# Optimization experiments

Hardware: AMD Instinct MI355X
Metric: run time of the kernel (lower is better)

The kernel has to match this reference:

```python
import jax, jax.numpy as jnp
import numpy as np

VOCAB_SIZES = [100003, 100019, 100043, 100049, 100057, 100069, 100103, 100109,
               100129, 100151, 100153, 100169, 100183, 100189, 100193, 100207]
OFFSETS = np.cumsum([0] + VOCAB_SIZES[:-1]).astype(np.int32)  # per-head offsets into shared table
B, S, G, C = 2, 2048, 4, 2048        # batch, seq, hc_mult branches, base_emb_dim
H, DH = 16, 64                        # total hash heads, dim_per_head
ENGRAM_DIM = H * DH                   # 1024 = num_orders * dim_per_ngram
K, DIL = 4, 3                         # conv kernel_size, dilation = max_ngram_size


def setup_inputs() -> dict:
  key = jax.random.key(0)
  ks = jax.random.split(key, 8)
  total_vocab = sum(VOCAB_SIZES)
  return {
      "hidden_states": jax.random.normal(ks[0], (B, S, G, C), jnp.float32),
      "hash_input_ids": jax.random.randint(ks[1], (B, S, H), 0, min(VOCAB_SIZES), jnp.int32),
      "emb_table": jax.random.normal(ks[2], (total_vocab, DH), jnp.float32) * 0.02,
      "key_w": jax.random.normal(ks[3], (G, ENGRAM_DIM, C), jnp.float32) / np.sqrt(ENGRAM_DIM),
      "key_b": jnp.zeros((G, C), jnp.float32),
      "k_scale": jnp.ones((G, C), jnp.float32) + 0.02 * jax.random.normal(ks[4], (G, C), jnp.float32),
      "q_scale": jnp.ones((G, C), jnp.float32) + 0.02 * jax.random.normal(ks[5], (G, C), jnp.float32),
      "value_w": jax.random.normal(ks[6], (ENGRAM_DIM, C), jnp.float32) / np.sqrt(ENGRAM_DIM),
      "value_b": jnp.zeros((C,), jnp.float32),
      "conv_scale": jnp.ones((G, C), jnp.float32),
      "conv_w": jax.random.normal(ks[7], (K, G * C), jnp.float32) * 0.25,  # depthwise taps
  }


def _rmsnorm(x, scale, eps):
  var = jnp.mean(jnp.square(x), axis=-1, keepdims=True)
  return x * jax.lax.rsqrt(var + eps) * scale


def reference(hidden_states, hash_input_ids, emb_table, key_w, key_b,
              k_scale, q_scale, value_w, value_b, conv_scale, conv_w):
  # 1. Retrieve: offset-shifted multi-head embedding gather
  ids = hash_input_ids + jnp.asarray(OFFSETS)            # (B,S,H)
  emb = emb_table[ids].reshape(B, S, ENGRAM_DIM)         # (B,S,H*DH)
  # 2. Gate: per-branch key projections + RMSNorms, signed-sqrt sigmoid gate
  keys = jnp.einsum('bse,geo->bsgo', emb, key_w) + key_b  # (B,S,G,C)
  k = _rmsnorm(keys, k_scale, 1e-6)
  q = _rmsnorm(hidden_states, q_scale, 1e-6)
  qk = jnp.einsum('bsgc,bsgc->bsg', q, k) / jnp.sqrt(jnp.float32(C))
  gate_logits = jnp.sqrt(jnp.maximum(jnp.abs(qk), 1e-6)) * jnp.sign(qk)
  gates = jax.nn.sigmoid(gate_logits)                    # (B,S,G)
  value = emb @ value_w + value_b                        # (B,S,C)
  v = gates[..., None] * value[:, :, None, :]            # (B,S,G,C)
  # 3. Mix: ShortConv = SiLU(depthwise causal dilated Conv1D(RMSNorm(v)))
  xn = _rmsnorm(v, conv_scale, 1e-5).reshape(B, S, G * C)
  pad = (K - 1) * DIL                                    # causal left pad = 9
  xp = jnp.pad(xn, ((0, 0), (pad, 0), (0, 0)))
  y = sum(xp[:, j * DIL:j * DIL + S, :] * conv_w[j] for j in range(K))
  y = jax.nn.silu(y).reshape(B, S, G, C)
  return v + y
```

## Files before the change

### kernel.cpp

```cpp
#include <hip/hip_runtime.h>
#include <cstdint>
#include <cstddef>

typedef __attribute__((ext_vector_type(8))) __bf16 bf16x8;
typedef __attribute__((ext_vector_type(4))) float f32x4;
typedef __attribute__((ext_vector_type(4))) unsigned short u16x4;
typedef __attribute__((ext_vector_type(8))) unsigned short u16x8;

static constexpr int Bz = 2, Sz = 2048, Gz = 4, Cz = 2048;
static constexpr int Hh = 16, EDz = 1024;
static constexpr int Tz = Bz * Sz;
static constexpr int NALL = Gz * Cz + Cz;

__constant__ int OFF16[16] = {0, 100003, 200022, 300065, 400114, 500171, 600240,
                              700343, 800452, 900581, 1000732, 1100885, 1201054,
                              1301237, 1401426, 1501619};

__device__ __forceinline__ float bf2f(unsigned short s) {
  union { unsigned u; float f; } x; x.u = ((unsigned)s) << 16; return x.f;
}
__device__ __forceinline__ unsigned short f2bf(float f) {
  union { float f; unsigned u; } x; x.f = f;
  unsigned r = x.u + 0x7fff + ((x.u >> 16) & 1);
  return (unsigned short)(r >> 16);
}

__global__ __launch_bounds__(256) void k_prep0(float* __restrict__ sums) {
  int i = blockIdx.x * 256 + threadIdx.x;
  if (i < 53248) sums[i] = 0.f;
}

__global__ __launch_bounds__(256) void k_prepw(const float* __restrict__ key_w,
                                               const float* __restrict__ value_w,
                                               unsigned short* __restrict__ Wt) {
  __shared__ float tile[32][33];
  const int mat = blockIdx.y;
  const int ot = blockIdx.x & 63, kt = blockIdx.x >> 6;
  const float* src = (mat < 4) ? (key_w + (size_t)mat * EDz * Cz) : value_w;
  const int tx = threadIdx.x & 31, ty = threadIdx.x >> 5;
#pragma unroll
  for (int i = 0; i < 4; i++)
    tile[ty + i * 8][tx] = src[(size_t)(kt * 32 + ty + i * 8) * Cz + ot * 32 + tx];
  __syncthreads();
#pragma unroll
  for (int i = 0; i < 4; i++)
    Wt[(size_t)(mat * Cz + ot * 32 + ty + i * 8) * EDz + kt * 32 + tx] =
        f2bf(tile[tx][ty + i * 8]);
}

__global__ __launch_bounds__(256) void k_gather(const int* __restrict__ ids,
                                                const float* __restrict__ table,
                                                unsigned short* __restrict__ emb) {
  const int t = blockIdx.x;
  const int tid = threadIdx.x;
  const int h = tid >> 4;
  const int d = (tid & 15) * 4;
  const long row = (long)(ids[t * Hh + h] + OFF16[h]);
  f32x4 v = *reinterpret_cast<const f32x4*>(table + row * 64 + d);
  u16x4 o;
#pragma unroll
  for (int i = 0; i < 4; i++) o[i] = f2bf(v[i]);
  *reinterpret_cast<u16x4*>(emb + (size_t)t * EDz + tid * 4) = o;
}

#define GEMM_BAR  asm volatile("s_barrier" ::: "memory")
#define GEMM_V4   asm volatile("s_waitcnt vmcnt(4)" ::: "memory")

__global__ __launch_bounds__(512, 2) void k_gemm8f(const unsigned short* __restrict__ A,
                                                   const unsigned short* __restrict__ Bw,
                                                   const float* __restrict__ hidden,
                                                   const float* __restrict__ key_b,
                                                   const float* __restrict__ value_b,
                                                   const float* __restrict__ q_scale,
                                                   const float* __restrict__ k_scale,
                                                   float* __restrict__ sums,
                                                   unsigned short* __restrict__ vbuf) {
  __shared__ unsigned short s_lds[65536];
  char* lds_c = (char*)s_lds;

  const int tid = threadIdx.x;
  const int wid = tid >> 6, lane = tid & 63;
  const int wr = wid >> 2, wc = wid & 3;

  const int bid = blockIdx.x;
  const int swz = (bid & 7) * 80 + (bid >> 3);
  const int bm = swz / 40, bn = swz % 40;
  const int m0 = bm * 256, n0 = bn * 256;

  int rq[2], kq[2];
#pragma unroll
  for (int q = 0; q < 2; q++) {
    int x = q * 8192 + wid * 1024 + lane * 16;
    int y = x ^ (((x >> 9) & 1) << 5);
    rq[q] = ((y >> 11) & 7) * 16 + ((y >> 6) & 15);
    kq[q] = ((y >> 10) & 1) * 32 + ((y >> 1) & 31);
  }
  const int rdb = (((lane & 15) << 6) + ((lane >> 4) << 4)) ^ (((lane >> 3) & 1) << 5);

  const unsigned short* Arow0 = A + (size_t)m0 * EDz;
  const unsigned short* Arow1 = A + (size_t)(m0 + 128) * EDz;
  const unsigned short* Brow0 = Bw + (size_t)n0 * EDz;
  const unsigned short* Brow1 = Bw + (size_t)(n0 + 128) * EDz;

  auto STAGE = [&](const unsigned short* grow, int ldsOff, int kt) {
#pragma unroll
    for (int q = 0; q < 2; q++) {
      const unsigned short* src = grow + (size_t)rq[q] * EDz + kt * 64 + kq[q];
      __builtin_amdgcn_global_load_lds(
          (const __attribute__((address_space(1))) void*)src,
          (__attribute__((address_space(3))) void*)(lds_c + ldsOff + q * 8192 + wid * 1024),
          16, 0, 0);
    }
  };

  f32x4 acc[8][4] = {};
  bf16x8 Af[4][2], Bl[2][2], Bh[2][2];

  auto RD_A = [&](int buf, int msel) {
    const char* p = lds_c + buf * 32768 + wr * 16384 + rdb;
#pragma unroll
    for (int m = 0; m < 4; m++)
#pragma unroll
      for (int ks = 0; ks < 2; ks++)
        Af[m][ks] = *reinterpret_cast<const bf16x8*>(p + (msel * 4 + m) * 2048 + ks * 1024);
  };
  auto RD_B = [&](int buf, int nsel, bf16x8 (&Bf)[2][2]) {
    const char* p = lds_c + 65536 + buf * 32768 + (wc >> 1) * 16384 + (wc & 1) * 8192 + rdb;
#pragma unroll
    for (int n = 0; n < 2; n++)
#pragma unroll
      for (int ks = 0; ks < 2; ks++)
        Bf[n][ks] = *reinterpret_cast<const bf16x8*>(p + (nsel * 2 + n) * 2048 + ks * 1024);
  };
  auto MM = [&](int msel, int nsel, bf16x8 (&Bf)[2][2]) {
    __builtin_amdgcn_s_setprio(1);
#pragma unroll
    for (int m = 0; m < 4; m++)
#pragma unroll
      for (int n = 0; n < 2; n++)
#pragma unroll
        for (int ks = 0; ks < 2; ks++)
          acc[msel * 4 + m][nsel * 2 + n] = __builtin_amdgcn_mfma_f32_16x16x32_bf16(
              Af[m][ks], Bf[n][ks], acc[msel * 4 + m][nsel * 2 + n], 0, 0, 0);
    __builtin_amdgcn_s_setprio(0);
  };

  STAGE(Arow0, 0,             0);
  STAGE(Arow1, 16384,         0);
  STAGE(Brow0, 65536,         0);
  STAGE(Brow1, 65536 + 16384, 0);
  STAGE(Brow0, 65536 + 32768,         1);
  STAGE(Brow1, 65536 + 32768 + 16384, 1);
  GEMM_V4;
  GEMM_BAR;

  for (int i = 0; i < 8; ++i) {
    const int o  = 2 * i + 1;
    const int t2 = (2 * i + 2 > 15) ? 15 : 2 * i + 2;
    const int t3 = (2 * i + 3 > 15) ? 15 : 2 * i + 3;
    RD_A(0, 0); RD_B(0, 0, Bl);
    STAGE(Arow0, 32768, o);
    GEMM_BAR; MM(0, 0, Bl); GEMM_BAR;
    RD_B(0, 1, Bh);
    STAGE(Arow1, 32768 + 16384, o);
    GEMM_BAR; MM(0, 1, Bh); GEMM_BAR;
    RD_A(0, 1);
    STAGE(Brow0, 65536, t2);
    GEMM_BAR; MM(1, 0, Bl); GEMM_BAR;
    STAGE(Brow1, 65536 + 16384, t2);
    GEMM_V4;
    GEMM_BAR; MM(1, 1, Bh); GEMM_BAR;
    RD_A(1, 0); RD_B(1, 0, Bl);
    STAGE(Arow0, 0, t2);
    GEMM_BAR; MM(0, 0, Bl); GEMM_BAR;
    RD_B(1, 1, Bh);
    STAGE(Arow1, 16384, t2);
    GEMM_BAR; MM(0, 1, Bh); GEMM_BAR;
    RD_A(1, 1);
    STAGE(Brow0, 65536 + 32768, t3);
    GEMM_BAR; MM(1, 0, Bl); GEMM_BAR;
    STAGE(Brow1, 65536 + 32768 + 16384, t3);
    GEMM_V4;
    GEMM_BAR; MM(1, 1, Bh); GEMM_BAR;
  }

  float* sum_q2  = sums;
  float* sum_k2  = sums + 16384;
  float* sum_qwk = sums + 32768;
  float* sum_v2  = sums + 49152;

  if (n0 < 8192) {
    const int g = n0 >> 11;
#pragma unroll
    for (int mrep = 0; mrep < 8; mrep++) {
      const int rowb = wr * 128 + mrep * 16 + (lane >> 4) * 4;
#pragma unroll
      for (int nrep = 0; nrep < 4; nrep++) {
        const int coll = wc * 64 + nrep * 16 + (lane & 15);
        const float kb = key_b[n0 + coll];
#pragma unroll
        for (int t = 0; t < 4; t++) {
          const int row = rowb + t;
          const int addr = (row * 512 + coll * 2) ^ ((row & 15) << 4);
          *reinterpret_cast<unsigned short*>(lds_c + addr) =
              f2bf(acc[mrep][nrep][t] + kb);
        }
      }
    }
    __syncthreads();
    const int wrow = wid * 32;
    const int lrow = lane >> 3;
    const int lsub = lane & 7;
#pragma unroll
    for (int rr = 0; rr < 4; rr++) {
      const int row = wrow + rr * 8 + lrow;
      const int grow = m0 + row;
      const float* hp = hidden + (size_t)grow * 8192 + n0;
      float a_k2 = 0.f, a_qwk = 0.f, a_q2 = 0.f;
#pragma unroll
      for (int c8 = 0; c8 < 4; c8++) {
        const int lc = c8 * 64 + lsub * 8;
        const int addr = (row * 512 + lc * 2) ^ ((row & 15) << 4);
        bf16x8 k8 = *reinterpret_cast<const bf16x8*>(lds_c + addr);
        f32x4 h0 = *reinterpret_cast<const f32x4*>(hp + lc);
        f32x4 h1 = *reinterpret_cast<const f32x4*>(hp + lc + 4);
        f32x4 qs0 = *reinterpret_cast<const f32x4*>(q_scale + n0 + lc);
        f32x4 qs1 = *reinterpret_cast<const f32x4*>(q_scale + n0 + lc + 4);
        f32x4 ks0 = *reinterpret_cast<const f32x4*>(k_scale + n0 + lc);
        f32x4 ks1 = *reinterpret_cast<const f32x4*>(k_scale + n0 + lc + 4);
#pragma unroll
        for (int i = 0; i < 8; i++) {
          const float kf = (float)k8[i];
          const float hf = (i < 4) ? h0[i] : h1[i - 4];
          const float wf = ((i < 4) ? qs0[i] : qs1[i - 4]) *
                           ((i < 4) ? ks0[i] : ks1[i - 4]);
          a_k2  += kf * kf;
          a_qwk += kf * hf * wf;
          a_q2  += hf * hf;
        }
      }
#pragma unroll
      for (int msk = 1; msk <= 4; msk <<= 1) {
        a_k2  += __shfl_xor(a_k2, msk);
        a_qwk += __shfl_xor(a_qwk, msk);
        a_q2  += __shfl_xor(a_q2, msk);
      }
      if (lsub == 0) {
        const int idx = grow * 4 + g;
        atomicAdd(&sum_k2[idx], a_k2);
        atomicAdd(&sum_qwk[idx], a_qwk);
        atomicAdd(&sum_q2[idx], a_q2);
      }
    }
  } else {
#pragma unroll
    for (int mrep = 0; mrep < 8; mrep++) {
      const int rowb = m0 + wr * 128 + mrep * 16 + (lane >> 4) * 4;
      float av2[4] = {0.f, 0.f, 0.f, 0.f};
#pragma unroll
      for (int nrep = 0; nrep < 4; nrep++) {
        const int vcol = n0 - 8192 + wc * 64 + nrep * 16 + (lane & 15);
        const float vb = value_b[vcol];
#pragma unroll
        for (int t = 0; t < 4; t++) {
          const float v = acc[mrep][nrep][t] + vb;
          av2[t] += v * v;
          vbuf[(size_t)(rowb + t) * 2048 + vcol] = f2bf(v);
        }
      }
#pragma unroll
      for (int t = 0; t < 4; t++) {
        float a = av2[t];
#pragma unroll
        for (int msk = 1; msk <= 8; msk <<= 1) a += __shfl_xor(a, msk);
        if ((lane & 15) == 0) atomicAdd(&sum_v2[rowb + t], a);
      }
    }
  }
}

__global__ __launch_bounds__(256) void k_gatefin(const float* __restrict__ sums,
                                                 float* __restrict__ gates,
                                                 float* __restrict__ rstd) {
  const int i = blockIdx.x * 256 + threadIdx.x;
  const float* sum_q2  = sums;
  const float* sum_k2  = sums + 16384;
  const float* sum_qwk = sums + 32768;
  const float* sum_v2  = sums + 49152;
  const int t = i >> 2;
  const float invC = 1.f / 2048.f;
  const float inv_sqrtC = 0.02209708691f;
  float rqv = rsqrtf(sum_q2[i] * invC + 1e-6f);
  float rkv = rsqrtf(sum_k2[i] * invC + 1e-6f);
  float qk = sum_qwk[i] * rqv * rkv * inv_sqrtC;
  float l = sqrtf(fmaxf(fabsf(qk), 1e-6f));
  l = (qk < 0.f) ? -l : l;
  float gate = 1.f / (1.f + expf(-l));
  gates[i] = gate;
  rstd[i] = rsqrtf(gate * gate * (sum_v2[t] * invC) + 1e-5f);
}

__global__ __launch_bounds__(256) void k_conv(const unsigned short* __restrict__ vbuf,
                                              const float* __restrict__ gates,
                                              const float* __restrict__ rstd,
                                              const float* __restrict__ conv_scale,
                                              const float* __restrict__ conv_w,
                                              float* __restrict__ out) {
  const int th = threadIdx.x;
  const int r = blockIdx.x % 3, seg = blockIdx.x / 3;
  const int bg = blockIdx.y;
  const int b = bg >> 2, g = bg & 3;
  const int c8 = th * 8;
  const int ch = g * Cz + c8;

  float cs[8], w0[8], w1[8], w2[8], w3[8];
#pragma unroll
  for (int q = 0; q < 2; q++) {
    f32x4 a = *reinterpret_cast<const f32x4*>(conv_scale + ch + q * 4);
    f32x4 t0 = *reinterpret_cast<const f32x4*>(conv_w + 0 * 8192 + ch + q * 4);
    f32x4 t1 = *reinterpret_cast<const f32x4*>(conv_w + 1 * 8192 + ch + q * 4);
    f32x4 t2 = *reinterpret_cast<const f32x4*>(conv_w + 2 * 8192 + ch + q * 4);
    f32x4 t3 = *reinterpret_cast<const f32x4*>(conv_w + 3 * 8192 + ch + q * 4);
#pragma unroll
    for (int i = 0; i < 4; i++) {
      cs[q * 4 + i] = a[i];
      w0[q * 4 + i] = t0[i]; w1[q * 4 + i] = t1[i];
      w2[q * 4 + i] = t2[i]; w3[q * 4 + i] = t3[i];
    }
  }

  const int s_begin = seg * 64, s_end = s_begin + 64;
  const int s0 = s_begin + ((r - s_begin) % 3 + 3) % 3;

  float p1[8], p2[8], p3[8];
  auto ldxn = [&](int s, float* dst) {
    if (s < 0) {
#pragma unroll
      for (int i = 0; i < 8; i++) dst[i] = 0.f;
      return;
    }
    const int t = b * Sz + s;
    const float grs = gates[t * 4 + g] * rstd[t * 4 + g];
    u16x8 raw = *reinterpret_cast<const u16x8*>(vbuf + (size_t)t * 2048 + c8);
#pragma unroll
    for (int i = 0; i < 8; i++) dst[i] = bf2f(raw[i]) * grs * cs[i];
  };
  ldxn(s0 - 3, p1); ldxn(s0 - 6, p2); ldxn(s0 - 9, p3);

  for (int s = s0; s < s_end; s += 3) {
    const int t = b * Sz + s;
    const float gate = gates[t * 4 + g];
    const float rsc = rstd[t * 4 + g];
    u16x8 raw = *reinterpret_cast<const u16x8*>(vbuf + (size_t)t * 2048 + c8);
    f32x4 o0, o1;
#pragma unroll
    for (int i = 0; i < 8; i++) {
      float v = bf2f(raw[i]) * gate;
      float xn = v * rsc * cs[i];
      float y = w3[i] * xn + w2[i] * p1[i] + w1[i] * p2[i] + w0[i] * p3[i];
      float sy = y / (1.f + expf(-y));
      float ov = v + sy;
      if (i < 4) o0[i] = ov; else o1[i - 4] = ov;
      p3[i] = p2[i]; p2[i] = p1[i]; p1[i] = xn;
    }
    float* op = out + (size_t)t * (Gz * Cz) + ch;
    *reinterpret_cast<f32x4*>(op) = o0;
    *reinterpret_cast<f32x4*>(op + 4) = o1;
  }
}

extern "C" void kernel_launch(void* const* d_in, const int* in_sizes, int n_in,
                              void* d_out, int out_size, void* d_ws, size_t ws_size,
                              hipStream_t stream) {
  const float* hidden     = (const float*)d_in[0];
  const int*   hashids    = (const int*)d_in[1];
  const float* table      = (const float*)d_in[2];
  const float* key_w      = (const float*)d_in[3];
  const float* key_b      = (const float*)d_in[4];
  const float* k_scale    = (const float*)d_in[5];
  const float* q_scale    = (const float*)d_in[6];
  const float* value_w    = (const float*)d_in[7];
  const float* value_b    = (const float*)d_in[8];
  const float* conv_scale = (const float*)d_in[9];
  const float* conv_w     = (const float*)d_in[10];
  float* out = (float*)d_out;
  char* ws = (char*)d_ws;

  unsigned short* emb  = (unsigned short*)(ws + 0);
  unsigned short* Wt   = (unsigned short*)(ws + 8388608);
  unsigned short* vbuf = (unsigned short*)(ws + 29360128);
  float* sums  = (float*)(ws + 46137344);
  float* gates = (float*)(ws + 46350336);
  float* rstd  = (float*)(ws + 46415872);

  k_prep0<<<dim3(208), dim3(256), 0, stream>>>(sums);
  k_prepw<<<dim3(2048, 5), dim3(256), 0, stream>>>(key_w, value_w, Wt);
  k_gather<<<dim3(Tz), dim3(256), 0, stream>>>(hashids, table, emb);
  k_gemm8f<<<dim3(640), dim3(512), 0, stream>>>(emb, Wt, hidden, key_b, value_b,
                                                q_scale, k_scale, sums, vbuf);
  k_gatefin<<<dim3(64), dim3(256), 0, stream>>>(sums, gates, rstd);
  k_conv<<<dim3(96, 8), dim3(256), 0, stream>>>(vbuf, gates, rstd, conv_scale, conv_w, out);
}
```

Before: 202.0 us.

## Fuse prep kernels into one launch and fold gate finalize into conv

Merges the sums-zeroing, weight transpose/convert and embedding gather kernels into a single launch that picks its role by block index. It also removes the separate gate-finalize kernel: each conv block now computes the gates and rstd values for its 64-row segment plus the 9-row causal halo into shared memory. The goal is to cut launch overhead and the intermediate gates/rstd round trip through global memory. In exchange, conv blocks recompute the gate values for halo rows and for each of the three residue blocks, and a block-wide barrier is added before the conv loop.

```diff
diff --git a/kernel.cpp b/kernel.cpp
--- a/kernel.cpp
+++ b/kernel.cpp
@@ -25,42 +25,44 @@
   return (unsigned short)(r >> 16);
 }
 
-__global__ __launch_bounds__(256) void k_prep0(float* __restrict__ sums) {
-  int i = blockIdx.x * 256 + threadIdx.x;
-  if (i < 53248) sums[i] = 0.f;
-}
-
-__global__ __launch_bounds__(256) void k_prepw(const float* __restrict__ key_w,
-                                               const float* __restrict__ value_w,
-                                               unsigned short* __restrict__ Wt) {
+__global__ __launch_bounds__(256) void k_prep(const float* __restrict__ key_w,
+                                              const float* __restrict__ value_w,
+                                              const float* __restrict__ table,
+                                              const int* __restrict__ ids,
+                                              unsigned short* __restrict__ Wt,
+                                              unsigned short* __restrict__ emb,
+                                              float* __restrict__ sums) {
+  const int b = blockIdx.x;
   __shared__ float tile[32][33];
-  const int mat = blockIdx.y;
-  const int ot = blockIdx.x & 63, kt = blockIdx.x >> 6;
-  const float* src = (mat < 4) ? (key_w + (size_t)mat * EDz * Cz) : value_w;
-  const int tx = threadIdx.x & 31, ty = threadIdx.x >> 5;
-#pragma unroll
-  for (int i = 0; i < 4; i++)
-    tile[ty + i * 8][tx] = src[(size_t)(kt * 32 + ty + i * 8) * Cz + ot * 32 + tx];
-  __syncthreads();
-#pragma unroll
-  for (int i = 0; i < 4; i++)
-    Wt[(size_t)(mat * Cz + ot * 32 + ty + i * 8) * EDz + kt * 32 + tx] =
-        f2bf(tile[tx][ty + i * 8]);
-}
-
-__global__ __launch_bounds__(256) void k_gather(const int* __restrict__ ids,
-                                                const float* __restrict__ table,
-                                                unsigned short* __restrict__ emb) {
-  const int t = blockIdx.x;
-  const int tid = threadIdx.x;
-  const int h = tid >> 4;
-  const int d = (tid & 15) * 4;
-  const long row = (long)(ids[t * Hh + h] + OFF16[h]);
-  f32x4 v = *reinterpret_cast<const f32x4*>(table + row * 64 + d);
-  u16x4 o;
-#pragma unroll
-  for (int i = 0; i < 4; i++) o[i] = f2bf(v[i]);
-  *reinterpret_cast<u16x4*>(emb + (size_t)t * EDz + tid * 4) = o;
+  if (b < 10240) {
+    const int mat = b / 2048;
+    const int inner = b - mat * 2048;
+    const int ot = inner & 63, kt = inner >> 6;
+    const float* src = (mat < 4) ? (key_w + (size_t)mat * EDz * Cz) : value_w;
+    const int tx = threadIdx.x & 31, ty = threadIdx.x >> 5;
+#pragma unroll
+    for (int i = 0; i < 4; i++)
+      tile[ty + i * 8][tx] = src[(size_t)(kt * 32 + ty + i * 8) * Cz + ot * 32 + tx];
+    __syncthreads();
+#pragma unroll
+    for (int i = 0; i < 4; i++)
+      Wt[(size_t)(mat * Cz + ot * 32 + ty + i * 8) * EDz + kt * 32 + tx] =
+          f2bf(tile[tx][ty + i * 8]);
+  } else if (b < 14336) {
+    const int t = b - 10240;
+    const int tid = threadIdx.x;
+    const int h = tid >> 4;
+    const int d = (tid & 15) * 4;
+    const long row = (long)(ids[t * Hh + h] + OFF16[h]);
+    f32x4 v = *reinterpret_cast<const f32x4*>(table + row * 64 + d);
+    u16x4 o;
+#pragma unroll
+    for (int i = 0; i < 4; i++) o[i] = f2bf(v[i]);
+    *reinterpret_cast<u16x4*>(emb + (size_t)t * EDz + tid * 4) = o;
+  } else {
+    const int i = (b - 14336) * 256 + threadIdx.x;
+    if (i < 53248) sums[i] = 0.f;
+  }
 }
 
 #define GEMM_BAR  asm volatile("s_barrier" ::: "memory")
@@ -279,30 +281,8 @@
   }
 }
 
-__global__ __launch_bounds__(256) void k_gatefin(const float* __restrict__ sums,
-                                                 float* __restrict__ gates,
-                                                 float* __restrict__ rstd) {
-  const int i = blockIdx.x * 256 + threadIdx.x;
-  const float* sum_q2  = sums;
-  const float* sum_k2  = sums + 16384;
-  const float* sum_qwk = sums + 32768;
-  const float* sum_v2  = sums + 49152;
-  const int t = i >> 2;
-  const float invC = 1.f / 2048.f;
-  const float inv_sqrtC = 0.02209708691f;
-  float rqv = rsqrtf(sum_q2[i] * invC + 1e-6f);
-  float rkv = rsqrtf(sum_k2[i] * invC + 1e-6f);
-  float qk = sum_qwk[i] * rqv * rkv * inv_sqrtC;
-  float l = sqrtf(fmaxf(fabsf(qk), 1e-6f));
-  l = (qk < 0.f) ? -l : l;
-  float gate = 1.f / (1.f + expf(-l));
-  gates[i] = gate;
-  rstd[i] = rsqrtf(gate * gate * (sum_v2[t] * invC) + 1e-5f);
-}
-
 __global__ __launch_bounds__(256) void k_conv(const unsigned short* __restrict__ vbuf,
-                                              const float* __restrict__ gates,
-                                              const float* __restrict__ rstd,
+                                              const float* __restrict__ sums,
                                               const float* __restrict__ conv_scale,
                                               const float* __restrict__ conv_w,
                                               float* __restrict__ out) {
@@ -312,6 +292,29 @@
   const int b = bg >> 2, g = bg & 3;
   const int c8 = th * 8;
   const int ch = g * Cz + c8;
+  const int s_begin = seg * 64, s_end = s_begin + 64;
+
+  __shared__ float g_lds[73], r_lds[73];
+  if (th < 73) {
+    const int s = s_begin - 9 + th;
+    if (s >= 0) {
+      const int t = b * Sz + s;
+      const int idx = t * 4 + g;
+      const float invC = 1.f / 2048.f;
+      const float inv_sqrtC = 0.02209708691f;
+      float rqv = rsqrtf(sums[idx] * invC + 1e-6f);
+      float rkv = rsqrtf(sums[16384 + idx] * invC + 1e-6f);
+      float qk = sums[32768 + idx] * rqv * rkv * inv_sqrtC;
+      float l = sqrtf(fmaxf(fabsf(qk), 1e-6f));
+      l = (qk < 0.f) ? -l : l;
+      float gate = 1.f / (1.f + expf(-l));
+      g_lds[th] = gate;
+      r_lds[th] = rsqrtf(gate * gate * (sums[49152 + t] * invC) + 1e-5f);
+    } else {
+      g_lds[th] = 0.f; r_lds[th] = 0.f;
+    }
+  }
+  __syncthreads();
 
   float cs[8], w0[8], w1[8], w2[8], w3[8];
 #pragma unroll
@@ -329,7 +332,6 @@
     }
   }
 
-  const int s_begin = seg * 64, s_end = s_begin + 64;
   const int s0 = s_begin + ((r - s_begin) % 3 + 3) % 3;
 
   float p1[8], p2[8], p3[8];
@@ -340,7 +342,8 @@
       return;
     }
     const int t = b * Sz + s;
-    const float grs = gates[t * 4 + g] * rstd[t * 4 + g];
+    const int li = s - s_begin + 9;
+    const float grs = g_lds[li] * r_lds[li];
     u16x8 raw = *reinterpret_cast<const u16x8*>(vbuf + (size_t)t * 2048 + c8);
 #pragma unroll
     for (int i = 0; i < 8; i++) dst[i] = bf2f(raw[i]) * grs * cs[i];
@@ -349,8 +352,9 @@
 
   for (int s = s0; s < s_end; s += 3) {
     const int t = b * Sz + s;
-    const float gate = gates[t * 4 + g];
-    const float rsc = rstd[t * 4 + g];
+    const int li = s - s_begin + 9;
+    const float gate = g_lds[li];
+    const float rsc = r_lds[li];
     u16x8 raw = *reinterpret_cast<const u16x8*>(vbuf + (size_t)t * 2048 + c8);
     f32x4 o0, o1;
 #pragma unroll
@@ -390,14 +394,10 @@
   unsigned short* Wt   = (unsigned short*)(ws + 8388608);
   unsigned short* vbuf = (unsigned short*)(ws + 29360128);
   float* sums  = (float*)(ws + 46137344);
-  float* gates = (float*)(ws + 46350336);
-  float* rstd  = (float*)(ws + 46415872);
-
-  k_prep0<<<dim3(208), dim3(256), 0, stream>>>(sums);
-  k_prepw<<<dim3(2048, 5), dim3(256), 0, stream>>>(key_w, value_w, Wt);
-  k_gather<<<dim3(Tz), dim3(256), 0, stream>>>(hashids, table, emb);
+
+  k_prep<<<dim3(14544), dim3(256), 0, stream>>>(key_w, value_w, table, hashids,
+                                                Wt, emb, sums);
   k_gemm8f<<<dim3(640), dim3(512), 0, stream>>>(emb, Wt, hidden, key_b, value_b,
                                                 q_scale, k_scale, sums, vbuf);
-  k_gatefin<<<dim3(64), dim3(256), 0, stream>>>(sums, gates, rstd);
-  k_conv<<<dim3(96, 8), dim3(256), 0, stream>>>(vbuf, gates, rstd, conv_scale, conv_w, out);
-}
+  k_conv<<<dim3(96, 8), dim3(256), 0, stream>>>(vbuf, sums, conv_scale, conv_w, out);
+}
```

Measured after the change: 193.9 us. 4.0% less time.
